# Optimization experiments

Measured on AMD Instinct MI355X. Metric: run time of the kernel, lower is better.

The kernel has to match this reference:

```python
import jax, jax.numpy as jnp
import numpy as np


def setup_inputs() -> dict:
    key = jax.random.key(0)
    k1, k2, k3 = jax.random.split(key, 3)
    n_way, n_shot, d, n_query = 5, 10, 1024, 16384
    n_support = n_way * n_shot
    train_imgs = jax.random.normal(k1, (n_support, d), dtype=jnp.float32)
    # one-hot labels: exactly n_shot examples per class (interleaved)
    cls = jnp.tile(jnp.arange(n_way), n_shot)  # [n_support]
    train_labels = jax.nn.one_hot(cls, n_way, dtype=jnp.int64)
    query_imgs = jax.random.normal(k2, (n_query, d), dtype=jnp.float32)
    query_labels = jax.random.randint(k3, (n_query,), 0, n_way)
    return {"train_imgs": train_imgs, "train_labels": train_labels,
            "query_imgs": query_imgs, "query_labels": query_labels}


def reference(train_imgs, train_labels, query_imgs, query_labels):
    # backbone = identity: imgs are already feature embeddings
    n_support, n_way = train_labels.shape
    n_shot = n_support // n_way  # static
    support = train_imgs                      # [n_support, d]
    query = query_imgs                        # [n_query, d]

    # group support features by class: [n_way, n_shot, d]
    cls = jnp.argmax(train_labels, axis=1)
    order = jnp.argsort(cls, stable=True)
    grouped = support[order].reshape(n_way, n_shot, -1)
    mats = jnp.swapaxes(grouped, 1, 2)        # [n_way, d, n_shot]

    # batched reduced SVD (torch.svd some=True -> full_matrices=False)
    U, _, _ = jnp.linalg.svd(mats, full_matrices=False)  # [n_way, d, n_shot]
    Uk = U[:, :, : n_shot - 1]                # [n_way, d, k]

    # projection of queries onto each class subspace: P = Uk Uk^T q
    coeff = jnp.einsum('wdk,qd->wkq', Uk, query)   # [n_way, k, n_query]
    proj = jnp.einsum('wdk,wkq->wqd', Uk, coeff)   # [n_way, n_query, d]
    dist = jnp.sum((query[None, :, :] - proj) ** 2, axis=-1)  # [n_way, n_query]

    logits = -dist.T                           # [n_query, n_way]
    # normalize=False in this configuration
    return jax.nn.log_softmax(logits, axis=1)
```

## Files before the change

### kernel.cpp

```cpp
#include <hip/hip_runtime.h>
#include <stdint.h>


typedef __attribute__((ext_vector_type(4))) float f32x4;
typedef __attribute__((ext_vector_type(8))) short s16x8;

#define WS_G_OFF    0
#define WS_GH_OFF   4096
#define WS_P_OFF    8192
#define WS_Z_OFF    262144

#define RDL(x, l) __uint_as_float(__builtin_amdgcn_readlane(__float_as_uint(x), (l)))

__device__ __forceinline__ unsigned short f2bf(float f) {
  unsigned int u = __float_as_uint(f);
  u += 0x7FFFu + ((u >> 16) & 1u);
  return (unsigned short)(u >> 16);
}

__device__ __forceinline__ bool labels_int64(const int* L) {
  int cnt = 0; bool oddz = true;
  #pragma unroll
  for (int t = 0; t < 20; ++t) {
    int v = L[t];
    if (t & 1) { if (v) oddz = false; }
    else       { if (v) cnt++; }
  }
  return oddz && (cnt == 2);
}

__device__ __forceinline__ int cls_of(const int* L, bool is64, int i) {
  int best = -0x7fffffff, c = 0;
  #pragma unroll
  for (int j = 0; j < 5; ++j) {
    int v = is64 ? L[i * 10 + 2 * j] : L[i * 5 + j];
    if (v > best) { best = v; c = j; }
  }
  return c;
}

__global__ __launch_bounds__(256) void dsn_prep(const float* __restrict__ support,
                                                const int* __restrict__ labels,
                                                double* __restrict__ G,
                                                unsigned short* __restrict__ P) {
  int b = blockIdx.x;
  bool is64 = labels_int64(labels);

  if (b < 69) {
    int wid  = b * 4 + (threadIdx.x >> 6);
    int lane = threadIdx.x & 63;
    if (wid >= 275) return;
    int w = wid / 55, p = wid % 55;
    int a = 0;
    while (p >= 10 - a) { p -= 10 - a; a++; }
    int bb = a + p;

    int myc = (lane < 50) ? cls_of(labels, is64, lane) : -1;
    unsigned long long mask = __ballot(lane < 50 && myc == w);

    unsigned long long m = mask;
    for (int i = 0; i < a; ++i) m &= m - 1;
    int ia = __ffsll((unsigned long long)m) - 1;
    m = mask;
    for (int i = 0; i < bb; ++i) m &= m - 1;
    int ib = __ffsll((unsigned long long)m) - 1;

    const float* A = support + ia * 1024;
    const float* B = support + ib * 1024;
    double acc = 0.0;
    #pragma unroll
    for (int i = 0; i < 16; ++i) {
      int d = lane + 64 * i;
      acc += (double)A[d] * (double)B[d];
    }
    #pragma unroll
    for (int off = 32; off > 0; off >>= 1) acc += __shfl_xor(acc, off);
    if (lane == 0) {
      G[(w * 10 + a) * 10 + bb] = acc;
      G[(w * 10 + bb) * 10 + a] = acc;
    }
  } else {
    int r = b - 69;
    int w = r >> 4, kk = r & 15;
    int t = threadIdx.x;
    unsigned short* Prow = P + r * 1024;
    if (kk >= 10) {
      #pragma unroll
      for (int j = 0; j < 4; ++j) Prow[t + 256 * j] = 0;
      return;
    }
    __shared__ int sid;
    if (t < 64) {
      int myc = (t < 50) ? cls_of(labels, is64, t) : -1;
      unsigned long long mask = __ballot(t < 50 && myc == w);
      if (t == 0) {
        unsigned long long m = mask;
        for (int z = 0; z < kk; ++z) m &= m - 1;
        sid = __ffsll(m) - 1;
      }
    }
    __syncthreads();
    const float* src = support + (size_t)sid * 1024;
    #pragma unroll
    for (int j = 0; j < 4; ++j) Prow[t + 256 * j] = f2bf(src[t + 256 * j]);
  }
}

__global__ __launch_bounds__(256) void dsn_zs(const float* __restrict__ query,
                                              const unsigned short* __restrict__ P,
                                              const double* __restrict__ G,
                                              float* __restrict__ Ghat,
                                              float* __restrict__ Z) {
  if (blockIdx.x < 5) {
    if (threadIdx.x >= 64) return;
    int w = blockIdx.x;
    int li = threadIdx.x;
    int rr = (li < 10) ? li : 0;
    const double* Gr = G + w * 100 + rr * 10;

    float o[10], g[10], h[10];
    #pragma unroll
    for (int j = 0; j < 10; ++j) {
      o[j] = (float)Gr[j];
      g[j] = o[j];
      h[j] = (li == j) ? 1.f : 0.f;
    }

    #pragma unroll
    for (int k = 0; k < 10; ++k) {
      float piv = 1.f / RDL(g[k], k);
      float pg[10], ph[10];
      #pragma unroll
      for (int j = 0; j < 10; ++j) {
        pg[j] = RDL(g[j], k) * piv;
        ph[j] = RDL(h[j], k) * piv;
      }
      float f = g[k];
      bool isk = (li == k);
      #pragma unroll
      for (int j = 0; j < 10; ++j) {
        g[j] = isk ? pg[j] : g[j] - f * pg[j];
        h[j] = isk ? ph[j] : h[j] - f * ph[j];
      }
    }

    float b[10];
    float d = h[0];
    #pragma unroll
    for (int k = 1; k < 10; ++k) d = (li == k) ? h[k] : d;
    float dm = RDL(d, 0);
    #pragma unroll
    for (int k = 1; k < 10; ++k) dm = fmaxf(dm, RDL(d, k));
    float rn = 1.f / dm;
    #pragma unroll
    for (int j = 0; j < 10; ++j) b[j] = h[j] * rn;

    #pragma unroll
    for (int sq = 0; sq < 7; ++sq) {
      float c[10];
      #pragma unroll
      for (int j = 0; j < 10; ++j) {
        float s = 0.f;
        #pragma unroll
        for (int k = 0; k < 10; ++k) s += b[k] * RDL(b[j], k);
        c[j] = s;
      }
      float dd = c[0];
      #pragma unroll
      for (int k = 1; k < 10; ++k) dd = (li == k) ? c[k] : dd;
      float m = RDL(dd, 0);
      #pragma unroll
      for (int k = 1; k < 10; ++k) m = fmaxf(m, RDL(dd, k));
      float rm = 1.f / m;
      #pragma unroll
      for (int j = 0; j < 10; ++j) b[j] = c[j] * rm;
    }

    float db = b[0];
    #pragma unroll
    for (int k = 1; k < 10; ++k) db = (li == k) ? b[k] : db;
    int jmx = 0;
    float bv = RDL(db, 0);
    #pragma unroll
    for (int k = 1; k < 10; ++k) {
      float t2 = RDL(db, k);
      if (t2 > bv) { bv = t2; jmx = k; }
    }
    float v = b[0];
    #pragma unroll
    for (int k = 1; k < 10; ++k) v = (jmx == k) ? b[k] : v;
    #pragma unroll
    for (int rf = 0; rf < 2; ++rf) {
      float nv = 0.f;
      #pragma unroll
      for (int k = 0; k < 10; ++k) nv += b[k] * RDL(v, k);
      v = nv;
    }

    float gv = 0.f;
    #pragma unroll
    for (int k = 0; k < 10; ++k) gv += o[k] * RDL(v, k);
    float tn = v * gv;
    float denom = RDL(tn, 0);
    #pragma unroll
    for (int k = 1; k < 10; ++k) denom += RDL(tn, k);
    float rden = 1.f / denom;
    if (li < 10) {
      #pragma unroll
      for (int j = 0; j < 10; ++j)
        Ghat[w * 100 + li * 10 + j] = h[j] - v * RDL(v, j) * rden;
    }
    return;
  }

  int wid  = (blockIdx.x - 5) * 4 + (threadIdx.x >> 6);
  int lane = threadIdx.x & 63;
  int q0   = wid * 16;
  int qrow = lane & 15;
  int kbase = (lane >> 4) * 8;

  const float* qp = query + (size_t)(q0 + qrow) * 1024 + kbase;
  const unsigned short* up = P + qrow * 1024 + kbase;

  f32x4 acc[5];
  #pragma unroll
  for (int w = 0; w < 5; ++w) acc[w] = (f32x4){0.f, 0.f, 0.f, 0.f};

  #pragma unroll 4
  for (int kt = 0; kt < 32; ++kt) {
    const float* qk = qp + kt * 32;
    f32x4 lo = *(const f32x4*)qk;
    f32x4 hi = *(const f32x4*)(qk + 4);
    s16x8 bf;
    bf[0] = (short)f2bf(lo[0]); bf[1] = (short)f2bf(lo[1]);
    bf[2] = (short)f2bf(lo[2]); bf[3] = (short)f2bf(lo[3]);
    bf[4] = (short)f2bf(hi[0]); bf[5] = (short)f2bf(hi[1]);
    bf[6] = (short)f2bf(hi[2]); bf[7] = (short)f2bf(hi[3]);
    const unsigned short* uk = up + kt * 32;
    #pragma unroll
    for (int w = 0; w < 5; ++w) {
      s16x8 av = *(const s16x8*)(uk + w * 16384);
      acc[w] = __builtin_amdgcn_mfma_f32_16x16x32_bf16(av, bf, acc[w], 0, 0, 0);
    }
  }

  int rowbase = (lane >> 4) * 4;
  #pragma unroll
  for (int w = 0; w < 5; ++w) {
    #pragma unroll
    for (int r = 0; r < 4; ++r)
      Z[(size_t)(w * 16 + rowbase + r) * 16384 + q0 + qrow] = acc[w][r];
  }
}

__global__ __launch_bounds__(256) void dsn_post(const float* __restrict__ Ghat,
                                                const float* __restrict__ Z,
                                                float* __restrict__ out) {
  __shared__ float Gh[500];
  int t = threadIdx.x;
  for (int i = t; i < 500; i += 256) Gh[i] = Ghat[i];
  __syncthreads();
  int q = blockIdx.x * 256 + t;

  float zv[50];
  #pragma unroll
  for (int w = 0; w < 5; ++w)
    #pragma unroll
    for (int s = 0; s < 10; ++s)
      zv[w * 10 + s] = Z[(size_t)(w * 16 + s) * 16384 + q];

  float sv[5];
  #pragma unroll
  for (int w = 0; w < 5; ++w) {
    float s = 0.f;
    #pragma unroll
    for (int i = 0; i < 10; ++i) {
      float gz = 0.f;
      #pragma unroll
      for (int j = 0; j < 10; ++j) gz += Gh[w * 100 + i * 10 + j] * zv[w * 10 + j];
      s += zv[w * 10 + i] * gz;
    }
    sv[w] = s;
  }
  float mx = fmaxf(fmaxf(fmaxf(sv[0], sv[1]), fmaxf(sv[2], sv[3])), sv[4]);
  float sum = 0.f;
  #pragma unroll
  for (int w = 0; w < 5; ++w) sum += expf(sv[w] - mx);
  float lse = mx + logf(sum);
  float* o = out + (size_t)q * 5;
  #pragma unroll
  for (int w = 0; w < 5; ++w) o[w] = sv[w] - lse;
}

extern "C" void kernel_launch(void* const* d_in, const int* in_sizes, int n_in,
                              void* d_out, int out_size, void* d_ws, size_t ws_size,
                              hipStream_t stream) {
  const float* support = (const float*)d_in[0];
  const int*   labels  = (const int*)d_in[1];
  const float* query   = (const float*)d_in[2];
  float* out = (float*)d_out;
  char* ws = (char*)d_ws;

  double*         G    = (double*)(ws + WS_G_OFF);
  float*          Ghat = (float*)(ws + WS_GH_OFF);
  unsigned short* P    = (unsigned short*)(ws + WS_P_OFF);
  float*          Z    = (float*)(ws + WS_Z_OFF);

  int nq = in_sizes[2] / 1024;
  int zs_blocks = nq / 64 + 5;
  int post_blocks = nq / 256;

  hipLaunchKernelGGL(dsn_prep, dim3(149), dim3(256), 0, stream, support, labels, G, P);
  hipLaunchKernelGGL(dsn_zs,   dim3(zs_blocks), dim3(256), 0, stream,
                     query, P, G, Ghat, Z);
  hipLaunchKernelGGL(dsn_post, dim3(post_blocks), dim3(256), 0, stream, Ghat, Z, out);
}
```

Baseline: 43.02 us.

## Fuse projection GEMM and post-processing into one kernel via shared-memory Z

```diff
diff --git a/kernel.cpp b/kernel.cpp
--- a/kernel.cpp
+++ b/kernel.cpp
@@ -6,9 +6,7 @@
 typedef __attribute__((ext_vector_type(8))) short s16x8;
 
 #define WS_G_OFF    0
-#define WS_GH_OFF   4096
 #define WS_P_OFF    8192
-#define WS_Z_OFF    262144
 
 #define RDL(x, l) __uint_as_float(__builtin_amdgcn_readlane(__float_as_uint(x), (l)))
 
@@ -106,15 +104,20 @@
   }
 }
 
-__global__ __launch_bounds__(256) void dsn_zs(const float* __restrict__ query,
-                                              const unsigned short* __restrict__ P,
-                                              const double* __restrict__ G,
-                                              float* __restrict__ Ghat,
-                                              float* __restrict__ Z) {
-  if (blockIdx.x < 5) {
-    if (threadIdx.x >= 64) return;
-    int w = blockIdx.x;
-    int li = threadIdx.x;
+__global__ __launch_bounds__(512) void dsn_fused(const float* __restrict__ query,
+                                                 const unsigned short* __restrict__ P,
+                                                 const double* __restrict__ G,
+                                                 float* __restrict__ out) {
+  __shared__ float Gh[500];
+  __shared__ float Zsh[80][132];
+
+  int t    = threadIdx.x;
+  int wave = t >> 6;
+  int lane = t & 63;
+
+  if (wave < 5) {
+    int w = wave;
+    int li = lane;
     int rr = (li < 10) ? li : 0;
     const double* Gr = G + w * 100 + rr * 10;
 
@@ -205,91 +208,88 @@
     #pragma unroll
     for (int k = 1; k < 10; ++k) denom += RDL(tn, k);
     float rden = 1.f / denom;
+    float vj[10];
+    #pragma unroll
+    for (int j = 0; j < 10; ++j) vj[j] = RDL(v, j);
     if (li < 10) {
       #pragma unroll
       for (int j = 0; j < 10; ++j)
-        Ghat[w * 100 + li * 10 + j] = h[j] - v * RDL(v, j) * rden;
-    }
-    return;
-  }
-
-  int wid  = (blockIdx.x - 5) * 4 + (threadIdx.x >> 6);
-  int lane = threadIdx.x & 63;
-  int q0   = wid * 16;
-  int qrow = lane & 15;
-  int kbase = (lane >> 4) * 8;
-
-  const float* qp = query + (size_t)(q0 + qrow) * 1024 + kbase;
-  const unsigned short* up = P + qrow * 1024 + kbase;
-
-  f32x4 acc[5];
-  #pragma unroll
-  for (int w = 0; w < 5; ++w) acc[w] = (f32x4){0.f, 0.f, 0.f, 0.f};
-
-  #pragma unroll 4
-  for (int kt = 0; kt < 32; ++kt) {
-    const float* qk = qp + kt * 32;
-    f32x4 lo = *(const f32x4*)qk;
-    f32x4 hi = *(const f32x4*)(qk + 4);
-    s16x8 bf;
-    bf[0] = (short)f2bf(lo[0]); bf[1] = (short)f2bf(lo[1]);
-    bf[2] = (short)f2bf(lo[2]); bf[3] = (short)f2bf(lo[3]);
-    bf[4] = (short)f2bf(hi[0]); bf[5] = (short)f2bf(hi[1]);
-    bf[6] = (short)f2bf(hi[2]); bf[7] = (short)f2bf(hi[3]);
-    const unsigned short* uk = up + kt * 32;
+        Gh[w * 100 + li * 10 + j] = h[j] - v * vj[j] * rden;
+    }
+  }
+
+  {
+    int q0   = blockIdx.x * 128 + wave * 16;
+    int qrow = lane & 15;
+    int kbase = (lane >> 4) * 8;
+
+    const float* qp = query + (size_t)(q0 + qrow) * 1024 + kbase;
+    const unsigned short* up = P + qrow * 1024 + kbase;
+
+    f32x4 acc[5];
+    #pragma unroll
+    for (int w = 0; w < 5; ++w) acc[w] = (f32x4){0.f, 0.f, 0.f, 0.f};
+
+    #pragma unroll 4
+    for (int kt = 0; kt < 32; ++kt) {
+      const float* qk = qp + kt * 32;
+      f32x4 lo = *(const f32x4*)qk;
+      f32x4 hi = *(const f32x4*)(qk + 4);
+      s16x8 bf;
+      bf[0] = (short)f2bf(lo[0]); bf[1] = (short)f2bf(lo[1]);
+      bf[2] = (short)f2bf(lo[2]); bf[3] = (short)f2bf(lo[3]);
+      bf[4] = (short)f2bf(hi[0]); bf[5] = (short)f2bf(hi[1]);
+      bf[6] = (short)f2bf(hi[2]); bf[7] = (short)f2bf(hi[3]);
+      const unsigned short* uk = up + kt * 32;
+      #pragma unroll
+      for (int w = 0; w < 5; ++w) {
+        s16x8 av = *(const s16x8*)(uk + w * 16384);
+        acc[w] = __builtin_amdgcn_mfma_f32_16x16x32_bf16(av, bf, acc[w], 0, 0, 0);
+      }
+    }
+
+    int rowbase = (lane >> 4) * 4;
+    int qcol = wave * 16 + qrow;
     #pragma unroll
     for (int w = 0; w < 5; ++w) {
-      s16x8 av = *(const s16x8*)(uk + w * 16384);
-      acc[w] = __builtin_amdgcn_mfma_f32_16x16x32_bf16(av, bf, acc[w], 0, 0, 0);
-    }
-  }
-
-  int rowbase = (lane >> 4) * 4;
-  #pragma unroll
-  for (int w = 0; w < 5; ++w) {
-    #pragma unroll
-    for (int r = 0; r < 4; ++r)
-      Z[(size_t)(w * 16 + rowbase + r) * 16384 + q0 + qrow] = acc[w][r];
-  }
-}
-
-__global__ __launch_bounds__(256) void dsn_post(const float* __restrict__ Ghat,
-                                                const float* __restrict__ Z,
-                                                float* __restrict__ out) {
-  __shared__ float Gh[500];
-  int t = threadIdx.x;
-  for (int i = t; i < 500; i += 256) Gh[i] = Ghat[i];
+      #pragma unroll
+      for (int r = 0; r < 4; ++r)
+        Zsh[w * 16 + rowbase + r][qcol] = acc[w][r];
+    }
+  }
   __syncthreads();
-  int q = blockIdx.x * 256 + t;
-
-  float zv[50];
-  #pragma unroll
-  for (int w = 0; w < 5; ++w)
-    #pragma unroll
-    for (int s = 0; s < 10; ++s)
-      zv[w * 10 + s] = Z[(size_t)(w * 16 + s) * 16384 + q];
-
-  float sv[5];
-  #pragma unroll
-  for (int w = 0; w < 5; ++w) {
-    float s = 0.f;
-    #pragma unroll
-    for (int i = 0; i < 10; ++i) {
-      float gz = 0.f;
-      #pragma unroll
-      for (int j = 0; j < 10; ++j) gz += Gh[w * 100 + i * 10 + j] * zv[w * 10 + j];
-      s += zv[w * 10 + i] * gz;
-    }
-    sv[w] = s;
-  }
-  float mx = fmaxf(fmaxf(fmaxf(sv[0], sv[1]), fmaxf(sv[2], sv[3])), sv[4]);
-  float sum = 0.f;
-  #pragma unroll
-  for (int w = 0; w < 5; ++w) sum += expf(sv[w] - mx);
-  float lse = mx + logf(sum);
-  float* o = out + (size_t)q * 5;
-  #pragma unroll
-  for (int w = 0; w < 5; ++w) o[w] = sv[w] - lse;
+
+  if (t < 128) {
+    int q = blockIdx.x * 128 + t;
+    float zv[50];
+    #pragma unroll
+    for (int w = 0; w < 5; ++w)
+      #pragma unroll
+      for (int s = 0; s < 10; ++s)
+        zv[w * 10 + s] = Zsh[w * 16 + s][t];
+
+    float sv[5];
+    #pragma unroll
+    for (int w = 0; w < 5; ++w) {
+      float s = 0.f;
+      #pragma unroll
+      for (int i = 0; i < 10; ++i) {
+        float gz = 0.f;
+        #pragma unroll
+        for (int j = 0; j < 10; ++j) gz += Gh[w * 100 + i * 10 + j] * zv[w * 10 + j];
+        s += zv[w * 10 + i] * gz;
+      }
+      sv[w] = s;
+    }
+    float mx = fmaxf(fmaxf(fmaxf(sv[0], sv[1]), fmaxf(sv[2], sv[3])), sv[4]);
+    float sum = 0.f;
+    #pragma unroll
+    for (int w = 0; w < 5; ++w) sum += expf(sv[w] - mx);
+    float lse = mx + logf(sum);
+    float* o = out + (size_t)q * 5;
+    #pragma unroll
+    for (int w = 0; w < 5; ++w) o[w] = sv[w] - lse;
+  }
 }
 
 extern "C" void kernel_launch(void* const* d_in, const int* in_sizes, int n_in,
@@ -301,17 +301,13 @@
   float* out = (float*)d_out;
   char* ws = (char*)d_ws;
 
-  double*         G    = (double*)(ws + WS_G_OFF);
-  float*          Ghat = (float*)(ws + WS_GH_OFF);
-  unsigned short* P    = (unsigned short*)(ws + WS_P_OFF);
-  float*          Z    = (float*)(ws + WS_Z_OFF);
+  double*         G = (double*)(ws + WS_G_OFF);
+  unsigned short* P = (unsigned short*)(ws + WS_P_OFF);
 
   int nq = in_sizes[2] / 1024;
-  int zs_blocks = nq / 64 + 5;
-  int post_blocks = nq / 256;
-
-  hipLaunchKernelGGL(dsn_prep, dim3(149), dim3(256), 0, stream, support, labels, G, P);
-  hipLaunchKernelGGL(dsn_zs,   dim3(zs_blocks), dim3(256), 0, stream,
-                     query, P, G, Ghat, Z);
-  hipLaunchKernelGGL(dsn_post, dim3(post_blocks), dim3(256), 0, stream, Ghat, Z, out);
-}
+  int fused_blocks = nq / 128;
+
+  hipLaunchKernelGGL(dsn_prep,  dim3(149), dim3(256), 0, stream, support, labels, G, P);
+  hipLaunchKernelGGL(dsn_fused, dim3(fused_blocks), dim3(512), 0, stream,
+                     query, P, G, out);
+}
```

Result: slower. 65.50 us (+52.3%).

## Fuse post-processing into projection kernel via LDS and a global readiness flag

Applied to the files above, without the earlier changes.

```diff
diff --git a/kernel.cpp b/kernel.cpp
--- a/kernel.cpp
+++ b/kernel.cpp
@@ -7,8 +7,8 @@
 
 #define WS_G_OFF    0
 #define WS_GH_OFF   4096
+#define WS_FLAG_OFF 6144
 #define WS_P_OFF    8192
-#define WS_Z_OFF    262144
 
 #define RDL(x, l) __uint_as_float(__builtin_amdgcn_readlane(__float_as_uint(x), (l)))
 
@@ -42,8 +42,13 @@
 __global__ __launch_bounds__(256) void dsn_prep(const float* __restrict__ support,
                                                 const int* __restrict__ labels,
                                                 double* __restrict__ G,
-                                                unsigned short* __restrict__ P) {
+                                                unsigned short* __restrict__ P,
+                                                int* __restrict__ flag) {
   int b = blockIdx.x;
+  if (b == 149) {
+    if (threadIdx.x == 0) *flag = 0;
+    return;
+  }
   bool is64 = labels_int64(labels);
 
   if (b < 69) {
@@ -110,7 +115,8 @@
                                               const unsigned short* __restrict__ P,
                                               const double* __restrict__ G,
                                               float* __restrict__ Ghat,
-                                              float* __restrict__ Z) {
+                                              int* __restrict__ flag,
+                                              float* __restrict__ out) {
   if (blockIdx.x < 5) {
     if (threadIdx.x >= 64) return;
     int w = blockIdx.x;
@@ -210,12 +216,21 @@
       for (int j = 0; j < 10; ++j)
         Ghat[w * 100 + li * 10 + j] = h[j] - v * RDL(v, j) * rden;
     }
+    if (li == 0) {
+      __threadfence();
+      atomicAdd(flag, 1);
+    }
     return;
   }
 
-  int wid  = (blockIdx.x - 5) * 4 + (threadIdx.x >> 6);
-  int lane = threadIdx.x & 63;
-  int q0   = wid * 16;
+  __shared__ float Zsh[4][80][16];
+  __shared__ float Ghs[500];
+
+  int t    = threadIdx.x;
+  int wave = t >> 6;
+  int lane = t & 63;
+  int gb   = blockIdx.x - 5;
+  int q0   = (gb * 4 + wave) * 16;
   int qrow = lane & 15;
   int kbase = (lane >> 4) * 8;
 
@@ -226,7 +241,7 @@
   #pragma unroll
   for (int w = 0; w < 5; ++w) acc[w] = (f32x4){0.f, 0.f, 0.f, 0.f};
 
-  #pragma unroll 4
+  #pragma unroll 8
   for (int kt = 0; kt < 32; ++kt) {
     const float* qk = qp + kt * 32;
     f32x4 lo = *(const f32x4*)qk;
@@ -249,47 +264,52 @@
   for (int w = 0; w < 5; ++w) {
     #pragma unroll
     for (int r = 0; r < 4; ++r)
-      Z[(size_t)(w * 16 + rowbase + r) * 16384 + q0 + qrow] = acc[w][r];
-  }
-}
-
-__global__ __launch_bounds__(256) void dsn_post(const float* __restrict__ Ghat,
-                                                const float* __restrict__ Z,
-                                                float* __restrict__ out) {
-  __shared__ float Gh[500];
-  int t = threadIdx.x;
-  for (int i = t; i < 500; i += 256) Gh[i] = Ghat[i];
+      Zsh[wave][w * 16 + rowbase + r][qrow] = acc[w][r];
+  }
+
+  if (t == 0) {
+    while (atomicAdd(flag, 0) < 5) __builtin_amdgcn_s_sleep(8);
+  }
   __syncthreads();
-  int q = blockIdx.x * 256 + t;
-
-  float zv[50];
-  #pragma unroll
-  for (int w = 0; w < 5; ++w)
-    #pragma unroll
-    for (int s = 0; s < 10; ++s)
-      zv[w * 10 + s] = Z[(size_t)(w * 16 + s) * 16384 + q];
-
-  float sv[5];
-  #pragma unroll
-  for (int w = 0; w < 5; ++w) {
-    float s = 0.f;
-    #pragma unroll
-    for (int i = 0; i < 10; ++i) {
-      float gz = 0.f;
-      #pragma unroll
-      for (int j = 0; j < 10; ++j) gz += Gh[w * 100 + i * 10 + j] * zv[w * 10 + j];
-      s += zv[w * 10 + i] * gz;
-    }
-    sv[w] = s;
-  }
-  float mx = fmaxf(fmaxf(fmaxf(sv[0], sv[1]), fmaxf(sv[2], sv[3])), sv[4]);
-  float sum = 0.f;
-  #pragma unroll
-  for (int w = 0; w < 5; ++w) sum += expf(sv[w] - mx);
-  float lse = mx + logf(sum);
-  float* o = out + (size_t)q * 5;
-  #pragma unroll
-  for (int w = 0; w < 5; ++w) o[w] = sv[w] - lse;
+  __threadfence();
+  if (t < 250) {
+    Ghs[t]       = atomicAdd(&Ghat[t], 0.f);
+    Ghs[t + 250] = atomicAdd(&Ghat[t + 250], 0.f);
+  }
+  __syncthreads();
+
+  if (t < 64) {
+    int q = gb * 64 + t;
+    int sl = t >> 4, col = t & 15;
+    float zv[50];
+    #pragma unroll
+    for (int w = 0; w < 5; ++w)
+      #pragma unroll
+      for (int s = 0; s < 10; ++s)
+        zv[w * 10 + s] = Zsh[sl][w * 16 + s][col];
+
+    float sv[5];
+    #pragma unroll
+    for (int w = 0; w < 5; ++w) {
+      float s = 0.f;
+      #pragma unroll
+      for (int i = 0; i < 10; ++i) {
+        float gz = 0.f;
+        #pragma unroll
+        for (int j = 0; j < 10; ++j) gz += Ghs[w * 100 + i * 10 + j] * zv[w * 10 + j];
+        s += zv[w * 10 + i] * gz;
+      }
+      sv[w] = s;
+    }
+    float mx = fmaxf(fmaxf(fmaxf(sv[0], sv[1]), fmaxf(sv[2], sv[3])), sv[4]);
+    float sum = 0.f;
+    #pragma unroll
+    for (int w = 0; w < 5; ++w) sum += expf(sv[w] - mx);
+    float lse = mx + logf(sum);
+    float* o = out + (size_t)q * 5;
+    #pragma unroll
+    for (int w = 0; w < 5; ++w) o[w] = sv[w] - lse;
+  }
 }
 
 extern "C" void kernel_launch(void* const* d_in, const int* in_sizes, int n_in,
@@ -303,15 +323,14 @@
 
   double*         G    = (double*)(ws + WS_G_OFF);
   float*          Ghat = (float*)(ws + WS_GH_OFF);
+  int*            flag = (int*)(ws + WS_FLAG_OFF);
   unsigned short* P    = (unsigned short*)(ws + WS_P_OFF);
-  float*          Z    = (float*)(ws + WS_Z_OFF);
 
   int nq = in_sizes[2] / 1024;
   int zs_blocks = nq / 64 + 5;
-  int post_blocks = nq / 256;
-
-  hipLaunchKernelGGL(dsn_prep, dim3(149), dim3(256), 0, stream, support, labels, G, P);
+
+  hipLaunchKernelGGL(dsn_prep, dim3(150), dim3(256), 0, stream,
+                     support, labels, G, P, flag);
   hipLaunchKernelGGL(dsn_zs,   dim3(zs_blocks), dim3(256), 0, stream,
-                     query, P, G, Ghat, Z);
-  hipLaunchKernelGGL(dsn_post, dim3(post_blocks), dim3(256), 0, stream, Ghat, Z, out);
-}
+                     query, P, G, Ghat, flag, out);
+}
```

Result: slower. 61.85 us (+43.8%).

## Split K across waves in Z projection kernel and speed up eigenvector iteration

Applied to the files above, without the earlier changes.

```diff
diff --git a/kernel.cpp b/kernel.cpp
--- a/kernel.cpp
+++ b/kernel.cpp
@@ -106,11 +106,11 @@
   }
 }
 
-__global__ __launch_bounds__(256) void dsn_zs(const float* __restrict__ query,
-                                              const unsigned short* __restrict__ P,
-                                              const double* __restrict__ G,
-                                              float* __restrict__ Ghat,
-                                              float* __restrict__ Z) {
+__global__ __launch_bounds__(256, 4) void dsn_zs(const float* __restrict__ query,
+                                                 const unsigned short* __restrict__ P,
+                                                 const double* __restrict__ G,
+                                                 float* __restrict__ Ghat,
+                                                 float* __restrict__ Z) {
   if (blockIdx.x < 5) {
     if (threadIdx.x >= 64) return;
     int w = blockIdx.x;
@@ -154,48 +154,41 @@
     float rn = 1.f / dm;
     #pragma unroll
     for (int j = 0; j < 10; ++j) b[j] = h[j] * rn;
-
-    #pragma unroll
-    for (int sq = 0; sq < 7; ++sq) {
-      float c[10];
-      #pragma unroll
-      for (int j = 0; j < 10; ++j) {
-        float s = 0.f;
-        #pragma unroll
-        for (int k = 0; k < 10; ++k) s += b[k] * RDL(b[j], k);
-        c[j] = s;
-      }
-      float dd = c[0];
-      #pragma unroll
-      for (int k = 1; k < 10; ++k) dd = (li == k) ? c[k] : dd;
-      float m = RDL(dd, 0);
-      #pragma unroll
-      for (int k = 1; k < 10; ++k) m = fmaxf(m, RDL(dd, k));
-      float rm = 1.f / m;
-      #pragma unroll
-      for (int j = 0; j < 10; ++j) b[j] = c[j] * rm;
-    }
-
-    float db = b[0];
-    #pragma unroll
-    for (int k = 1; k < 10; ++k) db = (li == k) ? b[k] : db;
+    float db = d * rn;
+
     int jmx = 0;
     float bv = RDL(db, 0);
+    float trB = bv;
     #pragma unroll
     for (int k = 1; k < 10; ++k) {
       float t2 = RDL(db, k);
+      trB += t2;
       if (t2 > bv) { bv = t2; jmx = k; }
     }
-    float v = b[0];
-    #pragma unroll
-    for (int k = 1; k < 10; ++k) v = (jmx == k) ? b[k] : v;
-    #pragma unroll
-    for (int rf = 0; rf < 2; ++rf) {
-      float nv = 0.f;
-      #pragma unroll
-      for (int k = 0; k < 10; ++k) nv += b[k] * RDL(v, k);
-      v = nv;
-    }
+    float sigma = (trB - bv) * (1.f / 9.f);
+    sigma = fminf(fmaxf(sigma, 0.f), 0.92f);
+    float rs = 1.f / (bv - sigma);
+
+    float x = (li == jmx) ? 1.f : 0.f;
+    #pragma unroll
+    for (int it = 0; it < 16; ++it) {
+      float xn = 0.f;
+      #pragma unroll
+      for (int k = 0; k < 10; ++k) xn += b[k] * RDL(x, k);
+      x = rs * (xn - sigma * x);
+    }
+    #pragma unroll
+    for (int it = 0; it < 2; ++it) {
+      float xn = 0.f;
+      #pragma unroll
+      for (int k = 0; k < 10; ++k) xn += b[k] * RDL(x, k);
+      float ax = fabsf(xn);
+      float mx = RDL(ax, 0);
+      #pragma unroll
+      for (int k = 1; k < 10; ++k) mx = fmaxf(mx, RDL(ax, k));
+      x = xn * (1.f / mx);
+    }
+    float v = x;
 
     float gv = 0.f;
     #pragma unroll
@@ -213,11 +206,14 @@
     return;
   }
 
-  int wid  = (blockIdx.x - 5) * 4 + (threadIdx.x >> 6);
-  int lane = threadIdx.x & 63;
-  int q0   = wid * 16;
+  __shared__ float Zsh[4][80][17];
+
+  int t    = threadIdx.x;
+  int wave = t >> 6;
+  int lane = t & 63;
+  int q0   = (blockIdx.x - 5) * 16;
   int qrow = lane & 15;
-  int kbase = (lane >> 4) * 8;
+  int kbase = wave * 256 + (lane >> 4) * 8;
 
   const float* qp = query + (size_t)(q0 + qrow) * 1024 + kbase;
   const unsigned short* up = P + qrow * 1024 + kbase;
@@ -226,8 +222,8 @@
   #pragma unroll
   for (int w = 0; w < 5; ++w) acc[w] = (f32x4){0.f, 0.f, 0.f, 0.f};
 
-  #pragma unroll 4
-  for (int kt = 0; kt < 32; ++kt) {
+  #pragma unroll
+  for (int kt = 0; kt < 8; ++kt) {
     const float* qk = qp + kt * 32;
     f32x4 lo = *(const f32x4*)qk;
     f32x4 hi = *(const f32x4*)(qk + 4);
@@ -249,7 +245,16 @@
   for (int w = 0; w < 5; ++w) {
     #pragma unroll
     for (int r = 0; r < 4; ++r)
-      Z[(size_t)(w * 16 + rowbase + r) * 16384 + q0 + qrow] = acc[w][r];
+      Zsh[wave][w * 16 + rowbase + r][qrow] = acc[w][r];
+  }
+  __syncthreads();
+
+  #pragma unroll
+  for (int idx = 0; idx < 5; ++idx) {
+    int e = t + idx * 256;
+    int s = e >> 4, c = e & 15;
+    float z = Zsh[0][s][c] + Zsh[1][s][c] + Zsh[2][s][c] + Zsh[3][s][c];
+    Z[(size_t)s * 16384 + q0 + c] = z;
   }
 }
 
@@ -307,7 +312,7 @@
   float*          Z    = (float*)(ws + WS_Z_OFF);
 
   int nq = in_sizes[2] / 1024;
-  int zs_blocks = nq / 64 + 5;
+  int zs_blocks = nq / 16 + 5;
   int post_blocks = nq / 256;
 
   hipLaunchKernelGGL(dsn_prep, dim3(149), dim3(256), 0, stream, support, labels, G, P);
```

Measured after the change: 42.92 us. Within noise of the previous version (-0.2%).
